# Kernel tuning notes

Measured on AMD Instinct MI355X. Metric: run time of the kernel, lower is better.

## Reference

```python
import jax, jax.numpy as jnp
import numpy as np

B, LQ, LKV = 32, 512, 512
SIZE, H = 512, 8
HD = SIZE // H
SCALE = 1.0 / np.sqrt(HD)
LN_EPS = 1e-5


def layer_norm(x, w, b):
    mu = jnp.mean(x, axis=-1, keepdims=True)
    var = jnp.mean(jnp.square(x - mu), axis=-1, keepdims=True)
    return (x - mu) * jax.lax.rsqrt(var + LN_EPS) * w + b


def setup_inputs() -> dict:
    key = jax.random.key(0)
    ks = jax.random.split(key, 8)
    s = 0.02
    return {
        "query": jax.random.normal(ks[0], (B, LQ, SIZE), jnp.float32),
        "key_value": jax.random.normal(ks[1], (B, LKV, SIZE), jnp.float32),
        "Wq": jax.random.normal(ks[2], (SIZE, SIZE), jnp.float32) * s,
        "bq": jnp.zeros((SIZE,), jnp.float32),
        "Wk": jax.random.normal(ks[3], (SIZE, SIZE), jnp.float32) * s,
        "bk": jnp.zeros((SIZE,), jnp.float32),
        "Wv": jax.random.normal(ks[4], (SIZE, SIZE), jnp.float32) * s,
        "bv": jnp.zeros((SIZE,), jnp.float32),
        "Wo": jax.random.normal(ks[5], (SIZE, SIZE), jnp.float32) * s,
        "bo": jnp.zeros((SIZE,), jnp.float32),
        "ln0_w": jnp.ones((SIZE,), jnp.float32),
        "ln0_b": jnp.zeros((SIZE,), jnp.float32),
        "ln1_w": jnp.ones((SIZE,), jnp.float32),
        "ln1_b": jnp.zeros((SIZE,), jnp.float32),
    }


def reference(query, key_value, Wq, bq, Wk, bk, Wv, bv, Wo, bo, ln0_w, ln0_b, ln1_w, ln1_b):
    b, lq, _ = query.shape
    lkv = key_value.shape[1]
    # projections
    q = query @ Wq.T + bq          # [B, Lq, SIZE]
    k = key_value @ Wk.T + bk      # [B, Lkv, SIZE]
    v = key_value @ Wv.T + bv
    # split heads: torch cat(split(head_size, 2), 0) == [B,L,H,HD] view with head axis separate
    qh = q.reshape(b, lq, H, HD)
    kh = k.reshape(b, lkv, H, HD)
    vh = v.reshape(b, lkv, H, HD)
    # attention scores [B, H, Lq, Lkv]
    A_ = jnp.einsum("bqhd,bkhd->bhqk", qh, kh) * SCALE
    # signed softmax: tanh(A_) * softmax(sqrt(A_^2 + 0.01)) over keys
    A = jnp.tanh(A_) * jax.nn.softmax(jnp.sqrt(jnp.square(A_) + 0.01), axis=-1)
    # residual q + attention output, merge heads back
    oh = qh + jnp.einsum("bhqk,bkhd->bqhd", A, vh)   # [B, Lq, H, HD]
    output = oh.reshape(b, lq, SIZE)
    output = layer_norm(output, ln0_w, ln0_b)
    output = output + jax.nn.relu(output @ Wo.T + bo)
    output = layer_norm(output, ln1_w, ln1_b)
    return output
```

## Files before the change

### kernel.cpp

```cpp
#include <hip/hip_runtime.h>

#define SIZE_D 512
#define HEADS  8
#define HDIM   64
#define BATCH  32
#define SEQ    512
#define SCALE_F 0.125f
#define NROWS  (BATCH * SEQ)

typedef __attribute__((ext_vector_type(8))) short bf16x8;
typedef __attribute__((ext_vector_type(4))) float f32x4;
typedef __attribute__((ext_vector_type(4))) unsigned int u32x4;

__device__ __forceinline__ unsigned short f2bf(float f) {
    union { float f; unsigned int u; } c{f};
    unsigned int x = c.u;
    x += 0x7fffu + ((x >> 16) & 1u);
    return (unsigned short)(x >> 16);
}
__device__ __forceinline__ float bf2f(unsigned short u) {
    union { unsigned int i; float f; } c;
    c.i = (unsigned int)u << 16;
    return c.f;
}
__device__ __forceinline__ void gload_lds16(const unsigned short* g, unsigned short* l) {
    __builtin_amdgcn_global_load_lds(
        (const __attribute__((address_space(1))) unsigned int*)g,
        (__attribute__((address_space(3))) unsigned int*)l, 16, 0, 0);
}

__global__ __launch_bounds__(256) void cvt_act(const float* __restrict__ q,
                                               const float* __restrict__ kv,
                                               unsigned short* __restrict__ dq,
                                               unsigned short* __restrict__ dkv) {
    const float* s = blockIdx.y ? kv : q;
    unsigned short* d = blockIdx.y ? dkv : dq;
    const int n = NROWS * SIZE_D;
    const int stride = gridDim.x * blockDim.x * 4;
    for (int i = (blockIdx.x * blockDim.x + threadIdx.x) * 4; i < n; i += stride) {
        const float4 v = *reinterpret_cast<const float4*>(s + i);
        ushort4 o;
        o.x = f2bf(v.x); o.y = f2bf(v.y); o.z = f2bf(v.z); o.w = f2bf(v.w);
        *reinterpret_cast<ushort4*>(d + i) = o;
    }
}

__global__ __launch_bounds__(256) void cvt_w4(const float* __restrict__ w0,
                                              const float* __restrict__ w1,
                                              const float* __restrict__ w2,
                                              const float* __restrict__ w3,
                                              unsigned short* __restrict__ d) {
    const float* srcs[4] = {w0, w1, w2, w3};
    const float* s = srcs[blockIdx.y];
    unsigned short* dst = d + (size_t)blockIdx.y * (SIZE_D * SIZE_D);
    const int n = SIZE_D * SIZE_D;
    const int stride = gridDim.x * blockDim.x * 4;
    for (int i = (blockIdx.x * blockDim.x + threadIdx.x) * 4; i < n; i += stride) {
        const float4 v = *reinterpret_cast<const float4*>(s + i);
        ushort4 o;
        o.x = f2bf(v.x); o.y = f2bf(v.y); o.z = f2bf(v.z); o.w = f2bf(v.w);
        *reinterpret_cast<ushort4*>(dst + i) = o;
    }
}

__global__ __launch_bounds__(256, 2) void gemm_proj3(const unsigned short* __restrict__ Qbf,
                                                     const unsigned short* __restrict__ KVbf,
                                                     const unsigned short* __restrict__ Wall,
                                                     const float* __restrict__ bq,
                                                     const float* __restrict__ bk,
                                                     const float* __restrict__ bv,
                                                     unsigned short* __restrict__ Qh,
                                                     unsigned short* __restrict__ Kh,
                                                     unsigned short* __restrict__ Vt) {
    __shared__ __align__(16) unsigned short Ad[2][128 * 64];
    __shared__ __align__(16) unsigned short Bd[2][128 * 64];

    const int tid  = threadIdx.x;
    const int wv   = tid >> 6;
    const int lane = tid & 63;
    const int y    = blockIdx.y;
    const int bm   = blockIdx.x * 128;
    const int bn   = y * 128;
    const int wr   = wv >> 1;
    const int wc   = wv & 1;

    const unsigned short* A = (y < 4) ? Qbf : KVbf;

    auto stage = [&](int buf, int t) {
        const int k0 = t * 64;
#pragma unroll
        for (int i = 0; i < 4; ++i) {
            const int o     = (wv * 32 + i * 8) * 128 + lane * 16;
            const int row   = o >> 7;
            const int inrow = (o & 127) ^ ((row & 7) << 4);
            const int col   = inrow >> 1;
            gload_lds16(A + (size_t)(bm + row) * SIZE_D + k0 + col, &Ad[buf][o >> 1]);
            gload_lds16(Wall + (size_t)(bn + row) * SIZE_D + k0 + col, &Bd[buf][o >> 1]);
        }
    };

    f32x4 acc[4][4];
#pragma unroll
    for (int mt = 0; mt < 4; ++mt)
#pragma unroll
        for (int nt = 0; nt < 4; ++nt) acc[mt][nt] = (f32x4){0.f, 0.f, 0.f, 0.f};

    stage(0, 0);
    __syncthreads();
    int cur = 0;

    for (int t = 0; t < 8; ++t) {
        if (t < 7) stage(cur ^ 1, t + 1);

        bf16x8 af[2][4], bfr[2][4];
#pragma unroll
        for (int kc = 0; kc < 2; ++kc) {
#pragma unroll
            for (int mt = 0; mt < 4; ++mt) {
                const int r = wr * 64 + mt * 16 + (lane & 15);
                int byte = r * 128 + kc * 64 + (lane >> 4) * 16;
                byte ^= (r & 7) << 4;
                af[kc][mt] = *reinterpret_cast<const bf16x8*>(
                    reinterpret_cast<const char*>(&Ad[cur][0]) + byte);
            }
#pragma unroll
            for (int nt = 0; nt < 4; ++nt) {
                const int r = wc * 64 + nt * 16 + (lane & 15);
                int byte = r * 128 + kc * 64 + (lane >> 4) * 16;
                byte ^= (r & 7) << 4;
                bfr[kc][nt] = *reinterpret_cast<const bf16x8*>(
                    reinterpret_cast<const char*>(&Bd[cur][0]) + byte);
            }
        }
#pragma unroll
        for (int kc = 0; kc < 2; ++kc)
#pragma unroll
            for (int mt = 0; mt < 4; ++mt)
#pragma unroll
                for (int nt = 0; nt < 4; ++nt)
                    acc[mt][nt] = __builtin_amdgcn_mfma_f32_16x16x32_bf16(
                        af[kc][mt], bfr[kc][nt], acc[mt][nt], 0, 0, 0);

        __syncthreads();
        cur ^= 1;
    }

    if (y < 8) {
        const float* bias = (y < 4) ? bq : bk;
        unsigned short* D = (y < 4) ? Qh : Kh;
        const int coff = (y < 4) ? 0 : 512;
#pragma unroll
        for (int nt = 0; nt < 4; ++nt) {
            const int colL = bn - coff + wc * 64 + nt * 16 + (lane & 15);
            const float bc = bias[colL];
            const int h = colL >> 6, dd = colL & 63;
#pragma unroll
            for (int mt = 0; mt < 4; ++mt) {
                const int row0 = bm + wr * 64 + mt * 16 + (lane >> 4) * 4;
#pragma unroll
                for (int r = 0; r < 4; ++r) {
                    const int row = row0 + r;
                    const int b_ = row >> 9, l = row & 511;
                    float z = acc[mt][nt][r] + bc;
                    if (y >= 4) z *= SCALE_F;
                    D[(((size_t)b_ * HEADS + h) * SEQ + l) * HDIM + dd] = f2bf(z);
                }
            }
        }
    } else {
#pragma unroll
        for (int nt = 0; nt < 4; ++nt) {
            const int c2 = bn - 1024 + wc * 64 + nt * 16 + (lane & 15);
            const float bc = bv[c2];
            const int hV = c2 >> 6, dV = c2 & 63;
#pragma unroll
            for (int mt = 0; mt < 4; ++mt) {
                const int row0 = bm + wr * 64 + mt * 16 + (lane >> 4) * 4;
                const int b_ = row0 >> 9, kv = row0 & 511;
                ushort4 pk;
                pk.x = f2bf(acc[mt][nt][0] + bc);
                pk.y = f2bf(acc[mt][nt][1] + bc);
                pk.z = f2bf(acc[mt][nt][2] + bc);
                pk.w = f2bf(acc[mt][nt][3] + bc);
                *reinterpret_cast<ushort4*>(
                    &Vt[(((size_t)b_ * HEADS + hV) * HDIM + dV) * SEQ + kv]) = pk;
            }
        }
    }
}

__global__ __launch_bounds__(256, 2) void attn_mfma(const unsigned short* __restrict__ Qh,
                                                    const unsigned short* __restrict__ Kh,
                                                    const unsigned short* __restrict__ Vt,
                                                    float* __restrict__ outq) {
    __shared__ __align__(16) unsigned short Kt[2][64 * 64];
    __shared__ __align__(16) unsigned short Vs[2][64 * 64];
    __shared__ __align__(16) unsigned short WL[4][64 * 64];

    const int tid  = threadIdx.x;
    const int wv   = tid >> 6;
    const int lane = tid & 63;
    const int bh   = blockIdx.x;
    const int half = blockIdx.y;
    const int b    = bh >> 3;
    const int h    = bh & 7;

    const unsigned short* Qb = Qh + (size_t)bh * (SEQ * HDIM);
    const unsigned short* Kb = Kh + (size_t)bh * (SEQ * HDIM);
    const unsigned short* Vb = Vt + (size_t)bh * (HDIM * SEQ);

    const int m0 = half * 256 + wv * 64;

    auto stageKV = [&](int buf, int t) {
        const int kv0 = t * 64;
#pragma unroll
        for (int i = 0; i < 2; ++i) {
            const int o   = i * 4096 + tid * 16;
            const int row = o >> 7;
            const int in  = (o & 127) ^ ((row & 7) << 4);
            gload_lds16(Kb + (size_t)(kv0 + row) * HDIM + (in >> 1), &Kt[buf][o >> 1]);
            gload_lds16(Vb + (size_t)row * SEQ + kv0 + (in >> 1), &Vs[buf][o >> 1]);
        }
    };

    bf16x8 qf[4][2];
#pragma unroll
    for (int mt = 0; mt < 4; ++mt)
#pragma unroll
        for (int kc = 0; kc < 2; ++kc) {
            const int m = m0 + mt * 16 + (lane & 15);
            union { u32x4 u; bf16x8 v; } cv;
            cv.u = *reinterpret_cast<const u32x4*>(
                Qb + (size_t)m * HDIM + kc * 32 + (lane >> 4) * 8);
            qf[mt][kc] = cv.v;
        }

    unsigned short* myW = &WL[wv][0];
    f32x4 oacc[4][4];
    float esum[4] = {0.f, 0.f, 0.f, 0.f};
#pragma unroll
    for (int mt = 0; mt < 4; ++mt)
#pragma unroll
        for (int x = 0; x < 4; ++x) oacc[mt][x] = (f32x4){0.f, 0.f, 0.f, 0.f};

    stageKV(0, 0);
    __syncthreads();
    int cur = 0;

    for (int t = 0; t < 8; ++t) {
        if (t < 7) stageKV(cur ^ 1, t + 1);

        f32x4 sacc[4][4];
#pragma unroll
        for (int nt = 0; nt < 4; ++nt)
#pragma unroll
            for (int mt = 0; mt < 4; ++mt) sacc[nt][mt] = (f32x4){0.f, 0.f, 0.f, 0.f};

#pragma unroll
        for (int kc = 0; kc < 2; ++kc) {
            bf16x8 kf[4];
#pragma unroll
            for (int nt = 0; nt < 4; ++nt) {
                const int kvl = nt * 16 + (lane & 15);
                int byte = kvl * 128 + kc * 64 + (lane >> 4) * 16;
                byte ^= (kvl & 7) << 4;
                kf[nt] = *reinterpret_cast<const bf16x8*>(
                    reinterpret_cast<const char*>(&Kt[cur][0]) + byte);
            }
#pragma unroll
            for (int nt = 0; nt < 4; ++nt)
#pragma unroll
                for (int mt = 0; mt < 4; ++mt)
                    sacc[nt][mt] = __builtin_amdgcn_mfma_f32_16x16x32_bf16(
                        kf[nt], qf[mt][kc], sacc[nt][mt], 0, 0, 0);
        }

#pragma unroll
        for (int nt = 0; nt < 4; ++nt)
#pragma unroll
            for (int mt = 0; mt < 4; ++mt) {
                float w[4];
#pragma unroll
                for (int r = 0; r < 4; ++r) {
                    const float s  = sacc[nt][mt][r];
                    const float a  = fminf(fabsf(s), 30.0f);
                    const float tt = __expf(a);
                    const float t2 = tt * tt;
                    const float u  = __builtin_amdgcn_sqrtf(fmaf(s, s, 0.01f));
                    const float dl = u - a;
                    const float ed = fmaf(dl, fmaf(dl, fmaf(dl, 0.16666667f, 0.5f), 1.0f), 1.0f);
                    const float eu = tt * ed;
                    esum[mt] += eu;
                    const float th = (t2 - 1.0f) * __builtin_amdgcn_rcpf(t2 + 1.0f);
                    w[r] = __builtin_copysignf(th * eu, s);
                }
                uint2 pk;
                pk.x = (__float_as_uint(w[1]) & 0xffff0000u) | (__float_as_uint(w[0]) >> 16);
                pk.y = (__float_as_uint(w[3]) & 0xffff0000u) | (__float_as_uint(w[2]) >> 16);
                int byte = (mt * 16 + (lane & 15)) * 128 + nt * 32 + (lane >> 4) * 8;
                byte ^= (lane & 7) << 4;
                *reinterpret_cast<uint2*>(reinterpret_cast<char*>(myW) + byte) = pk;
            }

#pragma unroll
        for (int kc2 = 0; kc2 < 2; ++kc2) {
            bf16x8 wf[4], vf[4];
#pragma unroll
            for (int mt = 0; mt < 4; ++mt) {
                const int row = mt * 16 + (lane & 15);
                int byte = row * 128 + kc2 * 64 + (lane >> 4) * 16;
                byte ^= (row & 7) << 4;
                wf[mt] = *reinterpret_cast<const bf16x8*>(
                    reinterpret_cast<const char*>(myW) + byte);
            }
#pragma unroll
            for (int dt = 0; dt < 4; ++dt) {
                const int d = dt * 16 + (lane & 15);
                int byte = d * 128 + kc2 * 64 + (lane >> 4) * 16;
                byte ^= (d & 7) << 4;
                vf[dt] = *reinterpret_cast<const bf16x8*>(
                    reinterpret_cast<const char*>(&Vs[cur][0]) + byte);
            }
#pragma unroll
            for (int mt = 0; mt < 4; ++mt)
#pragma unroll
                for (int dt = 0; dt < 4; ++dt)
                    oacc[mt][dt] = __builtin_amdgcn_mfma_f32_16x16x32_bf16(
                        wf[mt], vf[dt], oacc[mt][dt], 0, 0, 0);
        }

        __syncthreads();
        cur ^= 1;
    }

    float rden[4];
#pragma unroll
    for (int mt = 0; mt < 4; ++mt) {
        float e = esum[mt];
        e += __shfl_xor(e, 16);
        e += __shfl_xor(e, 32);
        rden[mt] = __builtin_amdgcn_rcpf(e);
    }
    float rr_[4][4];
#pragma unroll
    for (int mt = 0; mt < 4; ++mt)
#pragma unroll
        for (int r = 0; r < 4; ++r)
            rr_[mt][r] = __shfl(rden[mt], (lane >> 4) * 4 + r);

#pragma unroll
    for (int mt = 0; mt < 4; ++mt)
#pragma unroll
        for (int dt = 0; dt < 4; ++dt)
#pragma unroll
            for (int r = 0; r < 4; ++r) {
                const int m = m0 + mt * 16 + (lane >> 4) * 4 + r;
                const int d = dt * 16 + (lane & 15);
                const float qv = bf2f(Qb[(size_t)m * HDIM + d]);
                outq[((size_t)b * SEQ + m) * SIZE_D + h * HDIM + d] =
                    qv + oacc[mt][dt][r] * rr_[mt][r];
            }
}

__global__ __launch_bounds__(256) void ln0_bf16(const float* __restrict__ in,
                                                const float* __restrict__ w,
                                                const float* __restrict__ b,
                                                unsigned short* __restrict__ outb) {
    const int row = blockIdx.x;
    const int tid = threadIdx.x;
    const float2 x = *reinterpret_cast<const float2*>(&in[(size_t)row * SIZE_D + tid * 2]);

    float s  = x.x + x.y;
    float sq = x.x * x.x + x.y * x.y;
#pragma unroll
    for (int off = 32; off > 0; off >>= 1) {
        s  += __shfl_xor(s, off);
        sq += __shfl_xor(sq, off);
    }
    __shared__ float rs[4], rq[4];
    const int wv = tid >> 6;
    if ((tid & 63) == 0) { rs[wv] = s; rq[wv] = sq; }
    __syncthreads();
    s  = rs[0] + rs[1] + rs[2] + rs[3];
    sq = rq[0] + rq[1] + rq[2] + rq[3];

    const float mu  = s * (1.0f / SIZE_D);
    const float var = sq * (1.0f / SIZE_D) - mu * mu;
    const float rr  = rsqrtf(var + 1e-5f);

    const float2 wv2 = *reinterpret_cast<const float2*>(&w[tid * 2]);
    const float2 bv2 = *reinterpret_cast<const float2*>(&b[tid * 2]);
    ushort2 ob;
    ob.x = f2bf((x.x - mu) * rr * wv2.x + bv2.x);
    ob.y = f2bf((x.y - mu) * rr * wv2.y + bv2.y);
    *reinterpret_cast<ushort2*>(&outb[(size_t)row * SIZE_D + tid * 2]) = ob;
}

__global__ __launch_bounds__(512, 2) void oproj_ln(const unsigned short* __restrict__ X,
                                                   const unsigned short* __restrict__ W,
                                                   const float* __restrict__ bo,
                                                   const float* __restrict__ g1,
                                                   const float* __restrict__ b1,
                                                   float* __restrict__ out) {
    __shared__ __align__(16) unsigned short Ad[2][64 * 32];
    __shared__ __align__(16) unsigned short Bd[2][512 * 32];
    __shared__ float red[64][8][2];
    __shared__ float stat[64][2];

    const int tid  = threadIdx.x;
    const int wv   = tid >> 6;
    const int lane = tid & 63;
    const int bm   = blockIdx.x * 64;

    auto stage = [&](int buf, int t) {
        const int k0 = t * 32;
        if (tid < 256) {
            const int o   = tid * 16;
            const int row = o >> 6;
            const int in  = (o & 63) ^ (((row >> 1) & 3) << 4);
            gload_lds16(X + (size_t)(bm + row) * SIZE_D + k0 + (in >> 1), &Ad[buf][o >> 1]);
        }
#pragma unroll
        for (int i = 0; i < 4; ++i) {
            const int o   = i * 8192 + tid * 16;
            const int row = o >> 6;
            const int in  = (o & 63) ^ (((row >> 1) & 3) << 4);
            gload_lds16(W + (size_t)row * SIZE_D + k0 + (in >> 1), &Bd[buf][o >> 1]);
        }
    };

    f32x4 acc[4][4];
#pragma unroll
    for (int mt = 0; mt < 4; ++mt)
#pragma unroll
        for (int nt = 0; nt < 4; ++nt) acc[mt][nt] = (f32x4){0.f, 0.f, 0.f, 0.f};

    stage(0, 0);
    __syncthreads();
    int cur = 0;

    for (int t = 0; t < 16; ++t) {
        if (t < 15) stage(cur ^ 1, t + 1);

        bf16x8 af[4], bfr[4];
#pragma unroll
        for (int mt = 0; mt < 4; ++mt) {
            const int r = mt * 16 + (lane & 15);
            int byte = r * 64 + (lane >> 4) * 16;
            byte ^= ((r >> 1) & 3) << 4;
            af[mt] = *reinterpret_cast<const bf16x8*>(
                reinterpret_cast<const char*>(&Ad[cur][0]) + byte);
        }
#pragma unroll
        for (int nt = 0; nt < 4; ++nt) {
            const int r = wv * 64 + nt * 16 + (lane & 15);
            int byte = r * 64 + (lane >> 4) * 16;
            byte ^= ((r >> 1) & 3) << 4;
            bfr[nt] = *reinterpret_cast<const bf16x8*>(
                reinterpret_cast<const char*>(&Bd[cur][0]) + byte);
        }
#pragma unroll
        for (int mt = 0; mt < 4; ++mt)
#pragma unroll
            for (int nt = 0; nt < 4; ++nt)
                acc[mt][nt] = __builtin_amdgcn_mfma_f32_16x16x32_bf16(
                    af[mt], bfr[nt], acc[mt][nt], 0, 0, 0);

        __syncthreads();
        cur ^= 1;
    }

#pragma unroll
    for (int nt = 0; nt < 4; ++nt) {
        const int n  = wv * 64 + nt * 16 + (lane & 15);
        const float bc = bo[n];
#pragma unroll
        for (int mt = 0; mt < 4; ++mt) {
            const int row0 = bm + mt * 16 + (lane >> 4) * 4;
#pragma unroll
            for (int r = 0; r < 4; ++r) {
                const float R = bf2f(X[(size_t)(row0 + r) * SIZE_D + n]);
                acc[mt][nt][r] = R + fmaxf(acc[mt][nt][r] + bc, 0.0f);
            }
        }
    }

    float ps[4][4], pq[4][4];
#pragma unroll
    for (int mt = 0; mt < 4; ++mt)
#pragma unroll
        for (int r = 0; r < 4; ++r) {
            float s = 0.f, q = 0.f;
#pragma unroll
            for (int nt = 0; nt < 4; ++nt) {
                const float v = acc[mt][nt][r];
                s += v; q += v * v;
            }
#pragma unroll
            for (int off = 1; off <= 8; off <<= 1) {
                s += __shfl_xor(s, off);
                q += __shfl_xor(q, off);
            }
            ps[mt][r] = s; pq[mt][r] = q;
        }
    {
        const int mtw = (lane & 15) >> 2, rw = lane & 3;
        const int rowL = mtw * 16 + (lane >> 4) * 4 + rw;
        red[rowL][wv][0] = ps[mtw][rw];
        red[rowL][wv][1] = pq[mtw][rw];
    }
    __syncthreads();
    if (tid < 64) {
        float s = 0.f, q = 0.f;
#pragma unroll
        for (int w8 = 0; w8 < 8; ++w8) { s += red[tid][w8][0]; q += red[tid][w8][1]; }
        const float mu  = s * (1.0f / SIZE_D);
        const float var = q * (1.0f / SIZE_D) - mu * mu;
        stat[tid][0] = mu;
        stat[tid][1] = rsqrtf(var + 1e-5f);
    }
    __syncthreads();

#pragma unroll
    for (int nt = 0; nt < 4; ++nt) {
        const int n = wv * 64 + nt * 16 + (lane & 15);
        const float g = g1[n], bb = b1[n];
#pragma unroll
        for (int mt = 0; mt < 4; ++mt) {
#pragma unroll
            for (int r = 0; r < 4; ++r) {
                const int rowL = mt * 16 + (lane >> 4) * 4 + r;
                const float y = (acc[mt][nt][r] - stat[rowL][0]) * stat[rowL][1];
                out[(size_t)(bm + rowL) * SIZE_D + n] = y * g + bb;
            }
        }
    }
}

extern "C" void kernel_launch(void* const* d_in, const int* in_sizes, int n_in,
                              void* d_out, int out_size, void* d_ws, size_t ws_size,
                              hipStream_t stream) {
    const float* query = (const float*)d_in[0];
    const float* keyv  = (const float*)d_in[1];
    const float* Wq    = (const float*)d_in[2];
    const float* bq    = (const float*)d_in[3];
    const float* Wk    = (const float*)d_in[4];
    const float* bk    = (const float*)d_in[5];
    const float* Wv    = (const float*)d_in[6];
    const float* bv    = (const float*)d_in[7];
    const float* Wo    = (const float*)d_in[8];
    const float* bo    = (const float*)d_in[9];
    const float* ln0w  = (const float*)d_in[10];
    const float* ln0b  = (const float*)d_in[11];
    const float* ln1w  = (const float*)d_in[12];
    const float* ln1b  = (const float*)d_in[13];
    float* out = (float*)d_out;

    char* ws = (char*)d_ws;
    unsigned short* Qbf  = (unsigned short*)ws;
    unsigned short* KVbf = (unsigned short*)(ws + ((size_t)16 << 20));
    float*          qbuf = (float*)ws;
    unsigned short* Qh   = (unsigned short*)(ws + ((size_t)32 << 20));
    unsigned short* Xbf  = Qh;
    unsigned short* Kh   = (unsigned short*)(ws + ((size_t)48 << 20));
    unsigned short* Vt   = (unsigned short*)(ws + ((size_t)64 << 20));
    unsigned short* Wbf  = (unsigned short*)(ws + ((size_t)80 << 20));
    unsigned short* WoB  = Wbf + 786432;

    cvt_act<<<dim3(1024, 2), 256, 0, stream>>>(query, keyv, Qbf, KVbf);
    cvt_w4<<<dim3(64, 4), 256, 0, stream>>>(Wq, Wk, Wv, Wo, Wbf);

    gemm_proj3<<<dim3(128, 12), 256, 0, stream>>>(Qbf, KVbf, Wbf, bq, bk, bv, Qh, Kh, Vt);

    attn_mfma<<<dim3(BATCH * HEADS, 2), 256, 0, stream>>>(Qh, Kh, Vt, qbuf);

    ln0_bf16<<<NROWS, 256, 0, stream>>>(qbuf, ln0w, ln0b, Xbf);

    oproj_ln<<<NROWS / 64, 512, 0, stream>>>(Xbf, WoB, bo, ln1w, ln1b, out);
}
```

Before: 168.0 us.

## Keep attention weights in registers as MFMA operands, dropping LDS round-trip

The signed-softmax weights computed from the S=K·Q^T accumulators are packed directly into bf16x8 A-operands for the P·V MFMA, so the per-wave LDS scratch (WL) and its write/read are removed. The kv index order inside each operand is permuted, and V fragments are gathered from LDS as two 8-byte pieces to match that order. This saves LDS traffic and 32KB of shared memory, which may allow higher occupancy, at the cost of narrower V loads and more register pressure.

```diff
diff --git a/kernel.cpp b/kernel.cpp
--- a/kernel.cpp
+++ b/kernel.cpp
@@ -195,21 +195,20 @@
                                                     float* __restrict__ outq) {
     __shared__ __align__(16) unsigned short Kt[2][64 * 64];
     __shared__ __align__(16) unsigned short Vs[2][64 * 64];
-    __shared__ __align__(16) unsigned short WL[4][64 * 64];
 
     const int tid  = threadIdx.x;
     const int wv   = tid >> 6;
     const int lane = tid & 63;
     const int bh   = blockIdx.x;
-    const int half = blockIdx.y;
     const int b    = bh >> 3;
     const int h    = bh & 7;
+    const int g    = lane >> 4;
 
     const unsigned short* Qb = Qh + (size_t)bh * (SEQ * HDIM);
     const unsigned short* Kb = Kh + (size_t)bh * (SEQ * HDIM);
     const unsigned short* Vb = Vt + (size_t)bh * (HDIM * SEQ);
 
-    const int m0 = half * 256 + wv * 64;
+    const int m0 = blockIdx.y * 256 + wv * 64;
 
     auto stageKV = [&](int buf, int t) {
         const int kv0 = t * 64;
@@ -231,11 +230,10 @@
             const int m = m0 + mt * 16 + (lane & 15);
             union { u32x4 u; bf16x8 v; } cv;
             cv.u = *reinterpret_cast<const u32x4*>(
-                Qb + (size_t)m * HDIM + kc * 32 + (lane >> 4) * 8);
+                Qb + (size_t)m * HDIM + kc * 32 + g * 8);
             qf[mt][kc] = cv.v;
         }
 
-    unsigned short* myW = &WL[wv][0];
     f32x4 oacc[4][4];
     float esum[4] = {0.f, 0.f, 0.f, 0.f};
 #pragma unroll
@@ -262,7 +260,7 @@
 #pragma unroll
             for (int nt = 0; nt < 4; ++nt) {
                 const int kvl = nt * 16 + (lane & 15);
-                int byte = kvl * 128 + kc * 64 + (lane >> 4) * 16;
+                int byte = kvl * 128 + kc * 64 + g * 16;
                 byte ^= (kvl & 7) << 4;
                 kf[nt] = *reinterpret_cast<const bf16x8*>(
                     reinterpret_cast<const char*>(&Kt[cur][0]) + byte);
@@ -275,14 +273,15 @@
                         kf[nt], qf[mt][kc], sacc[nt][mt], 0, 0, 0);
         }
 
-#pragma unroll
-        for (int nt = 0; nt < 4; ++nt)
+        bf16x8 pa[2][4];
+#pragma unroll
+        for (int c = 0; c < 2; ++c)
 #pragma unroll
             for (int mt = 0; mt < 4; ++mt) {
-                float w[4];
-#pragma unroll
-                for (int r = 0; r < 4; ++r) {
-                    const float s  = sacc[nt][mt][r];
+                float w[8];
+#pragma unroll
+                for (int j = 0; j < 8; ++j) {
+                    const float s  = sacc[2 * c + (j >> 2)][mt][j & 3];
                     const float a  = fminf(fabsf(s), 30.0f);
                     const float tt = __expf(a);
                     const float t2 = tt * tt;
@@ -292,41 +291,41 @@
                     const float eu = tt * ed;
                     esum[mt] += eu;
                     const float th = (t2 - 1.0f) * __builtin_amdgcn_rcpf(t2 + 1.0f);
-                    w[r] = __builtin_copysignf(th * eu, s);
+                    w[j] = __builtin_copysignf(th * eu, s);
                 }
-                uint2 pk;
-                pk.x = (__float_as_uint(w[1]) & 0xffff0000u) | (__float_as_uint(w[0]) >> 16);
-                pk.y = (__float_as_uint(w[3]) & 0xffff0000u) | (__float_as_uint(w[2]) >> 16);
-                int byte = (mt * 16 + (lane & 15)) * 128 + nt * 32 + (lane >> 4) * 8;
-                byte ^= (lane & 7) << 4;
-                *reinterpret_cast<uint2*>(reinterpret_cast<char*>(myW) + byte) = pk;
-            }
-
-#pragma unroll
-        for (int kc2 = 0; kc2 < 2; ++kc2) {
-            bf16x8 wf[4], vf[4];
-#pragma unroll
-            for (int mt = 0; mt < 4; ++mt) {
-                const int row = mt * 16 + (lane & 15);
-                int byte = row * 128 + kc2 * 64 + (lane >> 4) * 16;
-                byte ^= (row & 7) << 4;
-                wf[mt] = *reinterpret_cast<const bf16x8*>(
-                    reinterpret_cast<const char*>(myW) + byte);
-            }
+                union { unsigned int u[4]; bf16x8 v; } pk;
+#pragma unroll
+                for (int p = 0; p < 4; ++p)
+                    pk.u[p] = (__float_as_uint(w[2 * p + 1]) & 0xffff0000u) |
+                              (__float_as_uint(w[2 * p]) >> 16);
+                pa[c][mt] = pk.v;
+            }
+
+#pragma unroll
+        for (int c = 0; c < 2; ++c) {
+            bf16x8 vf[4];
 #pragma unroll
             for (int dt = 0; dt < 4; ++dt) {
                 const int d = dt * 16 + (lane & 15);
-                int byte = d * 128 + kc2 * 64 + (lane >> 4) * 16;
-                byte ^= (d & 7) << 4;
-                vf[dt] = *reinterpret_cast<const bf16x8*>(
-                    reinterpret_cast<const char*>(&Vs[cur][0]) + byte);
+                const int swz = (d & 7) << 4;
+                const int rowb = d * 128;
+                uint2 lo = *reinterpret_cast<const uint2*>(
+                    reinterpret_cast<const char*>(&Vs[cur][0]) +
+                    (rowb + (((c * 32 + 4 * g) * 2) ^ swz)));
+                uint2 hi = *reinterpret_cast<const uint2*>(
+                    reinterpret_cast<const char*>(&Vs[cur][0]) +
+                    (rowb + (((c * 32 + 16 + 4 * g) * 2) ^ swz)));
+                union { unsigned int u[4]; bf16x8 v; } cvb;
+                cvb.u[0] = lo.x; cvb.u[1] = lo.y;
+                cvb.u[2] = hi.x; cvb.u[3] = hi.y;
+                vf[dt] = cvb.v;
             }
 #pragma unroll
             for (int mt = 0; mt < 4; ++mt)
 #pragma unroll
                 for (int dt = 0; dt < 4; ++dt)
                     oacc[mt][dt] = __builtin_amdgcn_mfma_f32_16x16x32_bf16(
-                        wf[mt], vf[dt], oacc[mt][dt], 0, 0, 0);
+                        pa[c][mt], vf[dt], oacc[mt][dt], 0, 0, 0);
         }
 
         __syncthreads();
@@ -346,7 +345,7 @@
     for (int mt = 0; mt < 4; ++mt)
 #pragma unroll
         for (int r = 0; r < 4; ++r)
-            rr_[mt][r] = __shfl(rden[mt], (lane >> 4) * 4 + r);
+            rr_[mt][r] = __shfl(rden[mt], g * 4 + r);
 
 #pragma unroll
     for (int mt = 0; mt < 4; ++mt)
@@ -354,7 +353,7 @@
         for (int dt = 0; dt < 4; ++dt)
 #pragma unroll
             for (int r = 0; r < 4; ++r) {
-                const int m = m0 + mt * 16 + (lane >> 4) * 4 + r;
+                const int m = m0 + mt * 16 + g * 4 + r;
                 const int d = dt * 16 + (lane & 15);
                 const float qv = bf2f(Qb[(size_t)m * HDIM + d]);
                 outq[((size_t)b * SEQ + m) * SIZE_D + h * HDIM + d] =
```

Result: no change. 166.4 us (-1.0%).
